# Kernel optimization log

Hardware: AMD Instinct MI355X
Metric: run time of the kernel (lower is better)

The kernel has to match this reference:

```python
import jax, jax.numpy as jnp
import numpy as np
from jax import lax

N = 100000      # nodes
E = 1600000     # edges
F_IN = 128      # nfeat
F_OUT = 32      # nhid


def _l2norm(v, eps=1e-12):
    return v / jnp.maximum(jnp.linalg.norm(v), eps)


def setup_inputs() -> dict:
    key = jax.random.key(0)
    k1, k2, k3, k4, k5 = jax.random.split(key, 5)
    x = jax.random.normal(k1, (N, F_IN), dtype=jnp.float32)
    edge_index = jax.random.randint(k2, (2, E), 0, N, dtype=jnp.int64)
    W = jax.random.normal(k3, (F_OUT, F_IN), dtype=jnp.float32) * (1.0 / np.sqrt(F_IN))
    bias = jax.random.normal(k4, (F_OUT,), dtype=jnp.float32) * 0.01
    prelu_a = jnp.full((1,), 0.25, dtype=jnp.float32)  # PReLU default init
    u_sn = jax.random.normal(k5, (F_OUT,), dtype=jnp.float32)
    return {"x": x, "edge_index": edge_index, "W": W, "bias": bias,
            "prelu_a": prelu_a, "u_sn": u_sn}


def _spectral_norm_weight(W, u):
    # one power iteration (torch default), u/v treated as buffers (no grad)
    v = lax.stop_gradient(_l2norm(W.T @ u))
    u2 = lax.stop_gradient(_l2norm(W @ v))
    sigma = jnp.dot(u2, W @ v)
    return W / sigma


def reference(x, edge_index, W, bias, prelu_a, u_sn):
    W_sn = _spectral_norm_weight(W, u_sn)
    # linear transform first (PyG GCNConv): [N, F_OUT]
    xw = x @ W_sn.T
    # add self loops
    loop = jnp.arange(N, dtype=edge_index.dtype)
    row = jnp.concatenate([edge_index[0], loop])  # source
    col = jnp.concatenate([edge_index[1], loop])  # target
    # symmetric normalization deg^{-1/2} A deg^{-1/2}, deg over targets
    deg = jax.ops.segment_sum(jnp.ones_like(col, dtype=xw.dtype), col, num_segments=N)
    dis = jnp.where(deg > 0, lax.rsqrt(deg), 0.0)
    norm = dis[row] * dis[col]                    # [E+N]
    # gather-scale-scatter aggregation
    msgs = xw[row] * norm[:, None]                # [E+N, F_OUT]
    out = jax.ops.segment_sum(msgs, col, num_segments=N)
    out = out + bias
    # PReLU with single shared slope
    a = prelu_a[0]
    return jnp.where(out >= 0, out, a * out)
```

## Files before the change

kernel.cpp:

```cpp
#include <hip/hip_runtime.h>
#include <hip/hip_fp16.h>

#define F_IN 128
#define F_OUT 32
#define PBLK 256
#define BSH 7
#define BMSK 127
#define MAXB 1024

__global__ __launch_bounds__(256) void k_hist(const int* __restrict__ col,
                                              int* __restrict__ M, int E_, int NB) {
    __shared__ int h[MAXB];
    int p = blockIdx.x, t = threadIdx.x;
    for (int b = t; b < NB; b += 256) h[b] = 0;
    __syncthreads();
    int epb = (E_ + PBLK - 1) / PBLK;
    int e0 = p * epb, e1 = min(e0 + epb, E_);
    for (int e = e0 + t; e < e1; e += 256)
        atomicAdd(&h[col[e] >> BSH], 1);
    __syncthreads();
    for (int b = t; b < NB; b += 256) M[(size_t)b * PBLK + p] = h[b];
}

__global__ __launch_bounds__(256) void k_scanA(int* __restrict__ M,
                                               int* __restrict__ total, int NB) {
    __shared__ int sd[256];
    int b = blockIdx.x, t = threadIdx.x;
    int v = M[(size_t)b * PBLK + t];
    sd[t] = v;
    __syncthreads();
    for (int o = 1; o < 256; o <<= 1) {
        int u = (t >= o) ? sd[t - o] : 0;
        __syncthreads();
        sd[t] += u;
        __syncthreads();
    }
    M[(size_t)b * PBLK + t] = sd[t] - v;
    if (t == 255) total[b] = sd[255];
}

__global__ __launch_bounds__(256) void k_scat1(
    const int* __restrict__ ei, const int* __restrict__ M,
    const int* __restrict__ total, int* __restrict__ base,
    unsigned* __restrict__ staging, int E_, int NB) {
    __shared__ int scur[MAXB];
    __shared__ int sd[256];
    int p = blockIdx.x, t = threadIdx.x;
    int C = (NB + 255) >> 8;
    int vals[4];
    int run = 0;
    for (int j = 0; j < C; ++j) {
        int b = t * C + j;
        int v = (b < NB) ? total[b] : 0;
        vals[j] = run;
        run += v;
    }
    int tsum = run;
    sd[t] = tsum;
    __syncthreads();
    for (int o = 1; o < 256; o <<= 1) {
        int u = (t >= o) ? sd[t - o] : 0;
        __syncthreads();
        sd[t] += u;
        __syncthreads();
    }
    int cb = sd[t] - tsum;
    for (int j = 0; j < C; ++j) {
        int b = t * C + j;
        if (b < NB) {
            int sb = cb + vals[j];
            scur[b] = sb + M[(size_t)b * PBLK + p];
            if (p == 0) base[b] = sb;
        }
    }
    if (p == 0 && t == 255) base[NB] = sd[255];
    __syncthreads();
    int epb = (E_ + PBLK - 1) / PBLK;
    int e0 = p * epb, e1 = min(e0 + epb, E_);
    const int* col = ei + E_;
    for (int e = e0 + t; e < e1; e += 256) {
        int c = col[e];
        int r = ei[e];
        int pos = atomicAdd(&scur[c >> BSH], 1);
        staging[pos] = ((unsigned)r << BSH) | (unsigned)(c & BMSK);
    }
}

__global__ __launch_bounds__(256) void k_sort2(
    const unsigned* __restrict__ staging, const int* __restrict__ base,
    int* __restrict__ esr, float* __restrict__ dis,
    int* __restrict__ cursor, int Nn, int E_, int NB) {
    __shared__ int hist[256];
    __shared__ int sd[256];
    __shared__ int lcur[256];
    int b = blockIdx.x, t = threadIdx.x;
    int nb0 = b << BSH;
    int nc = min(1 << BSH, Nn - nb0);
    hist[t] = 0;
    __syncthreads();
    int s0 = base[b], s1 = base[b + 1];
    for (int j = s0 + t; j < s1; j += 256)
        atomicAdd(&hist[staging[j] & BMSK], 1);
    __syncthreads();
    int h = hist[t];
    if (t < nc) dis[nb0 + t] = rsqrtf((float)h + 1.0f);
    sd[t] = h;
    __syncthreads();
    for (int o = 1; o < 256; o <<= 1) {
        int u = (t >= o) ? sd[t - o] : 0;
        __syncthreads();
        sd[t] += u;
        __syncthreads();
    }
    int excl = sd[t] - h;
    if (t < nc) cursor[nb0 + t] = s0 + excl;
    if (b == NB - 1 && t == 0) cursor[Nn] = E_;
    lcur[t] = s0 + excl;
    __syncthreads();
    for (int j = s0 + t; j < s1; j += 256) {
        unsigned v = staging[j];
        int pp = atomicAdd(&lcur[v & BMSK], 1);
        esr[pp] = (int)(v >> BSH);
    }
}

__global__ __launch_bounds__(256) void k1_xw(
    const float* __restrict__ x, const float* __restrict__ W,
    const float* __restrict__ u, const float* __restrict__ dis,
    __half* __restrict__ xwh, int Nn) {
    __shared__ float xs[128 * 65];
    __shared__ float wt[128 * 32];
    __shared__ float sv[F_IN];
    __shared__ float sr[F_IN];
    __shared__ float ssc;
    int t = threadIdx.x;

    if (t < F_IN) {
        float a = 0.f;
        for (int i = 0; i < F_OUT; ++i) a += W[i * F_IN + t] * u[i];
        sv[t] = a; sr[t] = a * a;
    }
    __syncthreads();
    for (int o = 64; o > 0; o >>= 1) {
        if (t < o) sr[t] += sr[t + o];
        __syncthreads();
    }
    if (t == 0) ssc = 1.0f / fmaxf(sqrtf(sr[0]), 1e-12f);
    __syncthreads();
    if (t < F_IN) sv[t] *= ssc;
    __syncthreads();
    if (t < F_OUT) {
        float a = 0.f;
        for (int j = 0; j < F_IN; ++j) a += W[t * F_IN + j] * sv[j];
        sr[t] = a * a;
    }
    __syncthreads();
    for (int o = 16; o > 0; o >>= 1) {
        if (t < o) sr[t] += sr[t + o];
        __syncthreads();
    }
    if (t == 0) ssc = 1.0f / fmaxf(sqrtf(sr[0]), 1e-30f);
    __syncthreads();
    float is = ssc;

    int rbase = blockIdx.x * 128;
    {
        int f = t >> 3;
        int kb = 16 * (t & 7);
        const float4* wrow = (const float4*)(W + (size_t)f * F_IN + kb);
#pragma unroll
        for (int j = 0; j < 4; ++j) {
            float4 w = wrow[j];
            int k = kb + 4 * j;
            wt[(k + 0) * 32 + f] = w.x * is;
            wt[(k + 1) * 32 + f] = w.y * is;
            wt[(k + 2) * 32 + f] = w.z * is;
            wt[(k + 3) * 32 + f] = w.w * is;
        }
    }

    int r0 = (t >> 3) * 4;
    int f0 = (t & 7) * 4;
    float4 acc0 = {0, 0, 0, 0}, acc1 = {0, 0, 0, 0};
    float4 acc2 = {0, 0, 0, 0}, acc3 = {0, 0, 0, 0};
    const float4* wt4 = (const float4*)wt;
    int fq = f0 >> 2;

    for (int kc = 0; kc < 2; ++kc) {
        __syncthreads();
        {
            int rr = t >> 4;
            int k0 = 4 * (t & 15);
#pragma unroll
            for (int pi = 0; pi < 8; ++pi) {
                int r = pi * 16 + rr;
                int grow = rbase + r;
                if (grow >= Nn) grow = Nn - 1;
                float4 v = *(const float4*)(x + (size_t)grow * F_IN + kc * 64 + k0);
                xs[r * 65 + k0 + 0] = v.x;
                xs[r * 65 + k0 + 1] = v.y;
                xs[r * 65 + k0 + 2] = v.z;
                xs[r * 65 + k0 + 3] = v.w;
            }
        }
        __syncthreads();
#pragma unroll 4
        for (int kk = 0; kk < 64; ++kk) {
            int k = kc * 64 + kk;
            float4 w = wt4[k * 8 + fq];
            float x0 = xs[(r0 + 0) * 65 + kk];
            float x1 = xs[(r0 + 1) * 65 + kk];
            float x2 = xs[(r0 + 2) * 65 + kk];
            float x3 = xs[(r0 + 3) * 65 + kk];
            acc0.x += x0 * w.x; acc0.y += x0 * w.y; acc0.z += x0 * w.z; acc0.w += x0 * w.w;
            acc1.x += x1 * w.x; acc1.y += x1 * w.y; acc1.z += x1 * w.z; acc1.w += x1 * w.w;
            acc2.x += x2 * w.x; acc2.y += x2 * w.y; acc2.z += x2 * w.z; acc2.w += x2 * w.w;
            acc3.x += x3 * w.x; acc3.y += x3 * w.y; acc3.z += x3 * w.z; acc3.w += x3 * w.w;
        }
    }
    int g0 = rbase + r0;
#pragma unroll
    for (int q = 0; q < 4; ++q) {
        int g = g0 + q;
        if (g < Nn) {
            float d = dis[g];
            float4 a = (q == 0) ? acc0 : (q == 1) ? acc1 : (q == 2) ? acc2 : acc3;
            ushort4 s;
            s.x = __half_as_ushort(__float2half(a.x * d));
            s.y = __half_as_ushort(__float2half(a.y * d));
            s.z = __half_as_ushort(__float2half(a.z * d));
            s.w = __half_as_ushort(__float2half(a.w * d));
            *(ushort4*)(xwh + (size_t)g * F_OUT + f0) = s;
        }
    }
}

__global__ __launch_bounds__(256) void k_gather(
    const int* __restrict__ esr, const int* __restrict__ cursor,
    const __half* __restrict__ xws, const float* __restrict__ dis,
    const float* __restrict__ bias, const float* __restrict__ pa,
    float* __restrict__ out, int Nn) {
    int t = threadIdx.x;
    int node = blockIdx.x * 16 + (t >> 4);
    if (node >= Nn) return;
    int f2 = t & 15;
    int start = cursor[node], end = cursor[node + 1];
    float accx = 0.f, accy = 0.f;
    for (int j0 = start; j0 < end; j0 += 16) {
        int idx = j0 + f2;
        int rf = (idx < end) ? esr[idx] : 0;
        int m = end - j0;
        if (m > 16) m = 16;
        int i = 0;
        for (; i + 4 <= m; i += 4) {
            int r0 = __shfl(rf, i + 0, 16);
            int r1 = __shfl(rf, i + 1, 16);
            int r2 = __shfl(rf, i + 2, 16);
            int r3 = __shfl(rf, i + 3, 16);
            float2 a0 = __half22float2(*((const __half2*)(xws + (size_t)r0 * F_OUT) + f2));
            float2 a1 = __half22float2(*((const __half2*)(xws + (size_t)r1 * F_OUT) + f2));
            float2 a2 = __half22float2(*((const __half2*)(xws + (size_t)r2 * F_OUT) + f2));
            float2 a3 = __half22float2(*((const __half2*)(xws + (size_t)r3 * F_OUT) + f2));
            accx += a0.x + a1.x + a2.x + a3.x;
            accy += a0.y + a1.y + a2.y + a3.y;
        }
        for (; i < m; ++i) {
            int r = __shfl(rf, i, 16);
            float2 a = __half22float2(*((const __half2*)(xws + (size_t)r * F_OUT) + f2));
            accx += a.x;
            accy += a.y;
        }
    }
    float dc = dis[node];
    float2 self = __half22float2(*((const __half2*)(xws + (size_t)node * F_OUT) + f2));
    float2 bi = *((const float2*)bias + f2);
    float a = pa[0];
    float vx = (accx + self.x) * dc + bi.x;
    float vy = (accy + self.y) * dc + bi.y;
    float2 o;
    o.x = (vx >= 0.f) ? vx : a * vx;
    o.y = (vy >= 0.f) ? vy : a * vy;
    *((float2*)(out + (size_t)node * F_OUT) + f2) = o;
}

__global__ void k0_specnorm(const float* __restrict__ W, const float* __restrict__ u,
                            float* __restrict__ Wsc) {
    __shared__ float v[F_IN];
    __shared__ float red[F_IN];
    __shared__ float scal;
    int t = threadIdx.x;
    float acc = 0.f;
    for (int i = 0; i < F_OUT; ++i) acc += W[i * F_IN + t] * u[i];
    v[t] = acc; red[t] = acc * acc;
    __syncthreads();
    if (t == 0) {
        float s = 0.f;
        for (int i = 0; i < F_IN; ++i) s += red[i];
        scal = 1.0f / fmaxf(sqrtf(s), 1e-12f);
    }
    __syncthreads();
    v[t] *= scal;
    __syncthreads();
    if (t < F_OUT) {
        float a2 = 0.f;
        for (int j = 0; j < F_IN; ++j) a2 += W[t * F_IN + j] * v[j];
        red[t] = a2 * a2;
    }
    __syncthreads();
    if (t == 0) {
        float s = 0.f;
        for (int i = 0; i < F_OUT; ++i) s += red[i];
        scal = 1.0f / fmaxf(sqrtf(s), 1e-30f);
    }
    __syncthreads();
    float is = scal;
    for (int i = 0; i < F_OUT; ++i)
        Wsc[i * F_IN + t] = W[i * F_IN + t] * is;
}

__global__ void k1_xw_f32(const float* __restrict__ x, const float* __restrict__ Wsc,
                          const float* __restrict__ dis, float* __restrict__ xw, int Nn) {
    int id = blockIdx.x * blockDim.x + threadIdx.x;
    if (id >= Nn * F_OUT) return;
    int r = id >> 5, f = id & 31;
    const float4* x4 = (const float4*)(x + (size_t)r * F_IN);
    const float4* w4 = (const float4*)(Wsc + (size_t)f * F_IN);
    float acc = 0.f;
#pragma unroll
    for (int k = 0; k < F_IN / 4; ++k) {
        float4 a = x4[k];
        float4 b = w4[k];
        acc += a.x * b.x + a.y * b.y + a.z * b.z + a.w * b.w;
    }
    xw[id] = acc * dis[r];
}

__global__ void k2_deg(const int* __restrict__ col, int* __restrict__ cnt, int E_) {
    int e = blockIdx.x * blockDim.x + threadIdx.x;
    if (e < E_) atomicAdd(&cnt[col[e]], 1);
}

__global__ void k3_dis(const int* __restrict__ cnt, float* __restrict__ dis, int Nn) {
    int i = blockIdx.x * blockDim.x + threadIdx.x;
    if (i < Nn) dis[i] = rsqrtf((float)cnt[i] + 1.0f);
}

__global__ void k4_scatter(const int* __restrict__ ei, const float* __restrict__ xws,
                           const float* __restrict__ dis, float* __restrict__ out, int E_) {
    int id = blockIdx.x * blockDim.x + threadIdx.x;
    if (id >= E_ * F_OUT) return;
    int e = id >> 5, f = id & 31;
    int r = ei[e];
    int c = ei[E_ + e];
    atomicAdd(&out[(size_t)c * F_OUT + f], xws[(size_t)r * F_OUT + f] * dis[c]);
}

__global__ void k5_epi(const float* __restrict__ xws, const float* __restrict__ dis,
                       const float* __restrict__ bias, const float* __restrict__ pa,
                       float* __restrict__ out, int Nn) {
    int id = blockIdx.x * blockDim.x + threadIdx.x;
    if (id >= Nn * F_OUT) return;
    int i = id >> 5, f = id & 31;
    float d = dis[i];
    float v = out[id] + xws[id] * d + bias[f];
    float a = pa[0];
    out[id] = (v >= 0.f) ? v : a * v;
}

extern "C" void kernel_launch(void* const* d_in, const int* in_sizes, int n_in,
                              void* d_out, int out_size, void* d_ws, size_t ws_size,
                              hipStream_t stream) {
    const float* x    = (const float*)d_in[0];
    const int*   ei   = (const int*)d_in[1];
    const float* W    = (const float*)d_in[2];
    const float* bias = (const float*)d_in[3];
    const float* pa   = (const float*)d_in[4];
    const float* u    = (const float*)d_in[5];

    int Nn = in_sizes[0] / F_IN;
    int E_ = in_sizes[1] / 2;
    float* out = (float*)d_out;

    int NB = (Nn + BMSK) >> BSH;

    size_t o = 0;
    __half*   xwh     = (__half*)d_ws;       o += (size_t)Nn * (F_OUT / 2);
    float*    dis     = (float*)d_ws + o;    o += Nn;
    int*      cursor  = (int*)d_ws + o;      o += Nn + 1;
    int*      M       = (int*)d_ws + o;      o += (size_t)NB * PBLK;
    int*      total   = (int*)d_ws + o;      o += NB;
    int*      base    = (int*)d_ws + o;      o += NB + 1;
    unsigned* staging = (unsigned*)d_ws + o; o += E_;
    int*      esr     = (int*)d_ws + o;      o += E_;
    bool big_ws = (ws_size >= o * sizeof(float)) && (NB <= MAXB);

    if (big_ws) {
        k_hist<<<PBLK, 256, 0, stream>>>(ei + E_, M, E_, NB);
        k_scanA<<<NB, 256, 0, stream>>>(M, total, NB);
        k_scat1<<<PBLK, 256, 0, stream>>>(ei, M, total, base, staging, E_, NB);
        k_sort2<<<NB, 256, 0, stream>>>(staging, base, esr, dis, cursor, Nn, E_, NB);
        k1_xw<<<(Nn + 127) / 128, 256, 0, stream>>>(x, W, u, dis, xwh, Nn);
        k_gather<<<(Nn + 15) / 16, 256, 0, stream>>>(esr, cursor, xwh, dis, bias, pa, out, Nn);
    } else {
        size_t o2 = 0;
        float* xw2  = (float*)d_ws;       o2 += (size_t)Nn * F_OUT;
        float* Wsc2 = (float*)d_ws + o2;  o2 += F_OUT * F_IN;
        float* dis2 = (float*)d_ws + o2;  o2 += Nn;
        int*   deg2 = (int*)d_ws + o2;    o2 += Nn;
        hipMemsetAsync(deg2, 0, (size_t)Nn * sizeof(int), stream);
        hipMemsetAsync(d_out, 0, (size_t)Nn * F_OUT * sizeof(float), stream);
        k0_specnorm<<<1, 128, 0, stream>>>(W, u, Wsc2);
        k2_deg<<<(E_ + 255) / 256, 256, 0, stream>>>(ei + E_, deg2, E_);
        k3_dis<<<(Nn + 255) / 256, 256, 0, stream>>>(deg2, dis2, Nn);
        int nT1 = Nn * F_OUT;
        k1_xw_f32<<<(nT1 + 255) / 256, 256, 0, stream>>>(x, Wsc2, dis2, xw2, Nn);
        int nT4 = E_ * F_OUT;
        k4_scatter<<<(nT4 + 255) / 256, 256, 0, stream>>>(ei, xw2, dis2, out, E_);
        k5_epi<<<(nT1 + 255) / 256, 256, 0, stream>>>(xw2, dis2, bias, pa, out, Nn);
    }
}
```

Measured before the change: 190.8 us.

## Widen gather to 8 lanes per node with 8-byte loads; double sort bucket size

The gather kernel now assigns 8 lanes per destination node instead of 16. Each lane loads 4 half values (uint2) per neighbor row and processes edges in fully unrolled groups of 8, so each block handles 32 nodes. The aim is more independent loads in flight per lane and more nodes per wavefront in this latency-bound gather, with float4 output stores. Separately, the counting-sort bucket width grows from 128 to 256 nodes, which halves the bucket count and the scan and histogram work. The catch is more work per bucket in the sort kernel.

After: 177.8 us. 6.8% less time.

```diff
diff --git a/kernel.cpp b/kernel.cpp
--- a/kernel.cpp
+++ b/kernel.cpp
@@ -4,9 +4,9 @@
 #define F_IN 128
 #define F_OUT 32
 #define PBLK 256
-#define BSH 7
-#define BMSK 127
-#define MAXB 1024
+#define BSH 8
+#define BMSK 255
+#define MAXB 512
 
 __global__ __launch_bounds__(256) void k_hist(const int* __restrict__ col,
                                               int* __restrict__ M, int E_, int NB) {
@@ -47,7 +47,7 @@
     __shared__ int sd[256];
     int p = blockIdx.x, t = threadIdx.x;
     int C = (NB + 255) >> 8;
-    int vals[4];
+    int vals[2];
     int run = 0;
     for (int j = 0; j < C; ++j) {
         int b = t * C + j;
@@ -235,52 +235,69 @@
     }
 }
 
+__device__ __forceinline__ void acc_row(const __half* xws, int r, int f4, float4& acc) {
+    uint2 raw = *((const uint2*)(xws + (size_t)r * F_OUT) + f4);
+    __half2 h0 = *reinterpret_cast<__half2*>(&raw.x);
+    __half2 h1 = *reinterpret_cast<__half2*>(&raw.y);
+    float2 fa = __half22float2(h0);
+    float2 fb = __half22float2(h1);
+    acc.x += fa.x; acc.y += fa.y; acc.z += fb.x; acc.w += fb.y;
+}
+
 __global__ __launch_bounds__(256) void k_gather(
     const int* __restrict__ esr, const int* __restrict__ cursor,
     const __half* __restrict__ xws, const float* __restrict__ dis,
     const float* __restrict__ bias, const float* __restrict__ pa,
     float* __restrict__ out, int Nn) {
     int t = threadIdx.x;
-    int node = blockIdx.x * 16 + (t >> 4);
+    int node = blockIdx.x * 32 + (t >> 3);
     if (node >= Nn) return;
-    int f2 = t & 15;
+    int f4 = t & 7;
     int start = cursor[node], end = cursor[node + 1];
-    float accx = 0.f, accy = 0.f;
-    for (int j0 = start; j0 < end; j0 += 16) {
-        int idx = j0 + f2;
+    float4 acc = {0, 0, 0, 0};
+    int j0 = start;
+    for (; j0 + 8 <= end; j0 += 8) {
+        int rf = esr[j0 + f4];
+        int r0 = __shfl(rf, 0, 8), r1 = __shfl(rf, 1, 8);
+        int r2 = __shfl(rf, 2, 8), r3 = __shfl(rf, 3, 8);
+        int r4 = __shfl(rf, 4, 8), r5 = __shfl(rf, 5, 8);
+        int r6 = __shfl(rf, 6, 8), r7 = __shfl(rf, 7, 8);
+        acc_row(xws, r0, f4, acc); acc_row(xws, r1, f4, acc);
+        acc_row(xws, r2, f4, acc); acc_row(xws, r3, f4, acc);
+        acc_row(xws, r4, f4, acc); acc_row(xws, r5, f4, acc);
+        acc_row(xws, r6, f4, acc); acc_row(xws, r7, f4, acc);
+    }
+    if (j0 < end) {
+        int idx = j0 + f4;
         int rf = (idx < end) ? esr[idx] : 0;
         int m = end - j0;
-        if (m > 16) m = 16;
-        int i = 0;
-        for (; i + 4 <= m; i += 4) {
-            int r0 = __shfl(rf, i + 0, 16);
-            int r1 = __shfl(rf, i + 1, 16);
-            int r2 = __shfl(rf, i + 2, 16);
-            int r3 = __shfl(rf, i + 3, 16);
-            float2 a0 = __half22float2(*((const __half2*)(xws + (size_t)r0 * F_OUT) + f2));
-            float2 a1 = __half22float2(*((const __half2*)(xws + (size_t)r1 * F_OUT) + f2));
-            float2 a2 = __half22float2(*((const __half2*)(xws + (size_t)r2 * F_OUT) + f2));
-            float2 a3 = __half22float2(*((const __half2*)(xws + (size_t)r3 * F_OUT) + f2));
-            accx += a0.x + a1.x + a2.x + a3.x;
-            accy += a0.y + a1.y + a2.y + a3.y;
-        }
-        for (; i < m; ++i) {
-            int r = __shfl(rf, i, 16);
-            float2 a = __half22float2(*((const __half2*)(xws + (size_t)r * F_OUT) + f2));
-            accx += a.x;
-            accy += a.y;
+        for (int i = 0; i < m; ++i) {
+            int r = __shfl(rf, i, 8);
+            acc_row(xws, r, f4, acc);
         }
     }
     float dc = dis[node];
-    float2 self = __half22float2(*((const __half2*)(xws + (size_t)node * F_OUT) + f2));
-    float2 bi = *((const float2*)bias + f2);
+    float4 self;
+    {
+        uint2 raw = *((const uint2*)(xws + (size_t)node * F_OUT) + f4);
+        __half2 h0 = *reinterpret_cast<__half2*>(&raw.x);
+        __half2 h1 = *reinterpret_cast<__half2*>(&raw.y);
+        float2 fa = __half22float2(h0);
+        float2 fb = __half22float2(h1);
+        self = make_float4(fa.x, fa.y, fb.x, fb.y);
+    }
+    float4 bi = *((const float4*)bias + f4);
     float a = pa[0];
-    float vx = (accx + self.x) * dc + bi.x;
-    float vy = (accy + self.y) * dc + bi.y;
-    float2 o;
-    o.x = (vx >= 0.f) ? vx : a * vx;
-    o.y = (vy >= 0.f) ? vy : a * vy;
-    *((float2*)(out + (size_t)node * F_OUT) + f2) = o;
+    float4 o;
+    o.x = (acc.x + self.x) * dc + bi.x;
+    o.y = (acc.y + self.y) * dc + bi.y;
+    o.z = (acc.z + self.z) * dc + bi.z;
+    o.w = (acc.w + self.w) * dc + bi.w;
+    o.x = (o.x >= 0.f) ? o.x : a * o.x;
+    o.y = (o.y >= 0.f) ? o.y : a * o.y;
+    o.z = (o.z >= 0.f) ? o.z : a * o.z;
+    o.w = (o.w >= 0.f) ? o.w : a * o.w;
+    *((float4*)(out + (size_t)node * F_OUT) + f4) = o;
 }
 
 __global__ void k0_specnorm(const float* __restrict__ W, const float* __restrict__ u,
@@ -400,7 +417,7 @@
         k_scat1<<<PBLK, 256, 0, stream>>>(ei, M, total, base, staging, E_, NB);
         k_sort2<<<NB, 256, 0, stream>>>(staging, base, esr, dis, cursor, Nn, E_, NB);
         k1_xw<<<(Nn + 127) / 128, 256, 0, stream>>>(x, W, u, dis, xwh, Nn);
-        k_gather<<<(Nn + 15) / 16, 256, 0, stream>>>(esr, cursor, xwh, dis, bias, pa, out, Nn);
+        k_gather<<<(Nn + 31) / 32, 256, 0, stream>>>(esr, cursor, xwh, dis, bias, pa, out, Nn);
     } else {
         size_t o2 = 0;
         float* xw2  = (float*)d_ws;       o2 += (size_t)Nn * F_OUT;
```
